# Kernel tuning notes

Hardware: AMD Instinct MI355X
Metric: run time of the kernel (lower is better)

The kernel has to match this reference:

```python
import jax, jax.numpy as jnp
import numpy as np

N = 100_000      # atom_count
E = 6_400_000    # number of (directed) edges, avg degree 64
BOX = 100.0      # simulation box edge length


def setup_inputs() -> dict:
    key = jax.random.key(0)
    k1, k2, k3 = jax.random.split(key, 3)
    pos = jax.random.uniform(k1, (N, 3), dtype=jnp.float32) * BOX
    src = jax.random.randint(k2, (E,), 0, N, dtype=jnp.int32)
    # offset in [1, N) guarantees dst != src (no zero-distance self edges)
    off = jax.random.randint(k3, (E,), 1, N, dtype=jnp.int32)
    dst = ((src + off) % N).astype(jnp.int32)
    edge_index = jnp.stack([src, dst], axis=0)  # [2, E]
    sigma = jnp.asarray(0.3, dtype=jnp.float32)
    epsilon = jnp.asarray(1.0, dtype=jnp.float32)
    return {"pos": pos, "sigma": sigma, "epsilon": epsilon, "edge_index": edge_index}


def _total_energy(pos, sigma, epsilon, src, dst):
    # r = edge_attr: per-edge distance, differentiable w.r.t. pos
    d = pos[src] - pos[dst]                      # [E, 3] gather + subtract
    r = jnp.sqrt(jnp.sum(d * d, axis=-1))        # [E]
    sr6 = (sigma / r) ** 6
    # potential_formula: 4*epsilon*((sigma/r)**12 - (sigma/r)**6)
    v_r = 4.0 * epsilon * (sr6 * sr6 - sr6)      # [E]
    return v_r.sum()


def reference(pos, sigma, epsilon, edge_index):
    src, dst = edge_index[0], edge_index[1]
    energy = _total_energy(pos, sigma, epsilon, src, dst)
    # afc: autograd force — grad of summed pair potential w.r.t. positions
    # (per-edge force scattered onto atoms by edge_index; grad does the
    #  gather-compute-scatter in one pass)
    pair_force = jax.grad(_total_energy, argnums=0)(pos, sigma, epsilon, src, dst)
    atom_force = -pair_force / 2.0               # /2: each pair counted twice
    return energy, atom_force
```

## Files before the change

kernel.cpp:

```cpp
#include <hip/hip_runtime.h>


#define NBINS      8
#define BIN_ATOMS  12800
#define BIN_F      (BIN_ATOMS * 3)
#define ROW_F      (NBINS * BIN_F)
#define BLOCK      1024
#define MAXCHUNKS  32

__global__ __launch_bounds__(BLOCK, 1) void pairforce_binned(
    const float* __restrict__ pos,
    const float* __restrict__ sigma_p,
    const float* __restrict__ eps_p,
    const int*   __restrict__ src,
    const int*   __restrict__ dst,
    float* __restrict__ frep,
    float* __restrict__ erep,
    int nEdges, int chunkEdges)
{
    extern __shared__ float sh[];
    const int t = threadIdx.x;
    const int b = blockIdx.x % NBINS;
    const int c = blockIdx.x / NBINS;

    for (int j = t; j < (BIN_F + 16) / 4; j += BLOCK)
        ((float4*)sh)[j] = make_float4(0.f, 0.f, 0.f, 0.f);
    __syncthreads();

    const float sigma = sigma_p[0];
    const float eps   = eps_p[0];
    const float sig2  = sigma * sigma;
    const int binStart = b * BIN_ATOMS;

    const int start = c * chunkEdges;
    const int end   = min(start + chunkEdges, nEdges);

    const int4* src4 = (const int4*)src;
    const int4* dst4 = (const int4*)dst;

    float ev = 0.0f;

    for (int i4 = (start >> 2) + t; i4 < (end >> 2); i4 += BLOCK) {
        const int4 s4 = src4[i4];
        const int4 d4 = dst4[i4];
        #pragma unroll
        for (int k = 0; k < 4; ++k) {
            const int s = (k == 0) ? s4.x : (k == 1) ? s4.y : (k == 2) ? s4.z : s4.w;
            const int d = (k == 0) ? d4.x : (k == 1) ? d4.y : (k == 2) ? d4.z : d4.w;
            const unsigned ls = (unsigned)(s - binStart);
            const unsigned ld = (unsigned)(d - binStart);
            const bool hs = ls < BIN_ATOMS;
            const bool hd = ld < BIN_ATOMS;
            if (hs | hd) {
                const float dx = pos[3 * s + 0] - pos[3 * d + 0];
                const float dy = pos[3 * s + 1] - pos[3 * d + 1];
                const float dz = pos[3 * s + 2] - pos[3 * d + 2];
                const float r2     = dx * dx + dy * dy + dz * dz;
                const float inv_r2 = 1.0f / r2;
                const float s2     = sig2 * inv_r2;
                const float sr6    = s2 * s2 * s2;
                const float sr12   = sr6 * sr6;
                const float fs = 12.0f * eps * (2.0f * sr12 - sr6) * inv_r2;
                const float fx = fs * dx;
                const float fy = fs * dy;
                const float fz = fs * dz;
                if (hs) {
                    atomicAdd(&sh[3 * ls + 0],  fx);
                    atomicAdd(&sh[3 * ls + 1],  fy);
                    atomicAdd(&sh[3 * ls + 2],  fz);
                    ev += 4.0f * eps * (sr12 - sr6);
                }
                if (hd) {
                    atomicAdd(&sh[3 * ld + 0], -fx);
                    atomicAdd(&sh[3 * ld + 1], -fy);
                    atomicAdd(&sh[3 * ld + 2], -fz);
                }
            }
        }
    }

    #pragma unroll
    for (int off = 32; off > 0; off >>= 1)
        ev += __shfl_down(ev, off, 64);
    if ((t & 63) == 0) sh[BIN_F + (t >> 6)] = ev;
    __syncthreads();

    float4* outSeg = (float4*)(frep + (size_t)c * ROW_F + (size_t)b * BIN_F);
    for (int j = t; j < BIN_F / 4; j += BLOCK)
        outSeg[j] = ((float4*)sh)[j];

    if (t == 0) {
        float e = 0.f;
        #pragma unroll
        for (int w = 0; w < 16; ++w) e += sh[BIN_F + w];
        erep[blockIdx.x] = e;
    }
}

__global__ __launch_bounds__(256) void pairforce_reduce(
    const float* __restrict__ frep,
    const float* __restrict__ erep,
    float* __restrict__ out,
    int n3, int nChunks, int nPart)
{
    const int i = blockIdx.x * 256 + threadIdx.x;
    if (i < n3) {
        float acc = 0.f;
        for (int c = 0; c < nChunks; ++c)
            acc += frep[(size_t)c * ROW_F + i];
        out[1 + i] = acc;
    }
    if (blockIdx.x == gridDim.x - 1) {
        float e = 0.f;
        for (int j = threadIdx.x; j < nPart; j += 256) e += erep[j];
        #pragma unroll
        for (int off = 32; off > 0; off >>= 1) e += __shfl_down(e, off, 64);
        __shared__ float ep[4];
        if ((threadIdx.x & 63) == 0) ep[threadIdx.x >> 6] = e;
        __syncthreads();
        if (threadIdx.x == 0) out[0] = ep[0] + ep[1] + ep[2] + ep[3];
    }
}

extern "C" void kernel_launch(void* const* d_in, const int* in_sizes, int n_in,
                              void* d_out, int out_size, void* d_ws, size_t ws_size,
                              hipStream_t stream)
{
    const float* pos     = (const float*)d_in[0];
    const float* sigma_p = (const float*)d_in[1];
    const float* eps_p   = (const float*)d_in[2];
    const int*   edge    = (const int*)d_in[3];

    const int nEdges = in_sizes[3] / 2;
    const int* src = edge;
    const int* dst = edge + nEdges;

    const int n3 = out_size - 1;

    const size_t rowBytes = (size_t)ROW_F * sizeof(float);
    int nChunks = (int)((ws_size - 4096) / rowBytes);
    if (nChunks > MAXCHUNKS) nChunks = MAXCHUNKS;
    if (nChunks < 1) nChunks = 1;

    const int chunkEdges = (((nEdges + nChunks - 1) / nChunks) + 3) & ~3;

    float* frep = (float*)d_ws;
    float* erep = frep + (size_t)nChunks * ROW_F;

    const size_t shbytes = (size_t)(BIN_F + 16) * sizeof(float);

    const int grid1 = nChunks * NBINS;
    pairforce_binned<<<grid1, BLOCK, shbytes, stream>>>(
        pos, sigma_p, eps_p, src, dst, frep, erep, nEdges, chunkEdges);

    const int grid2 = (n3 + 255) / 256;
    pairforce_reduce<<<grid2, 256, 0, stream>>>(
        frep, erep, (float*)d_out, n3, nChunks, nChunks * NBINS);
}
```

Measured before the change: 313.1 us.

## Replace atomic binned accumulation with counting-sort of edge records per atom class

Adds a multi-kernel pipeline: per-wave histogram of edge endpoints into bins and classes, a three-stage prefix scan, placement of encoded records, then a per-thread accumulation where each thread owns an atom class so shared-memory force sums need no atomics. Positions are repacked into float4 to make gathers single loads. It is meant to remove the shared-memory atomic contention and the redundant edge scans across 8 bins of the old kernel. In exchange it adds several launches, a low-parallelism count/place phase with serialized vote loops, and extra record traffic.

```diff
diff --git a/kernel.cpp b/kernel.cpp
--- a/kernel.cpp
+++ b/kernel.cpp
@@ -1,12 +1,308 @@
 #include <hip/hip_runtime.h>
 
+
+#define NBIN   32
+#define BA     3200
+#define NCLS   128
+#define LBK    (NBIN * NCLS)
+#define NSEG   512
+#define CBLK   64
+#define NB_TOT (NSEG * LBK)
+#define NROW   8
+#define ROW_F  307200
 
 #define NBINS      8
 #define BIN_ATOMS  12800
 #define BIN_F      (BIN_ATOMS * 3)
-#define ROW_F      (NBINS * BIN_F)
 #define BLOCK      1024
 #define MAXCHUNKS  32
+
+__device__ __forceinline__ unsigned nt_load_u(const unsigned* p) {
+    return __builtin_nontemporal_load(p);
+}
+
+
+__device__ __forceinline__ void vote_count(volatile unsigned* vh,
+                                           volatile unsigned* vote,
+                                           int lane, int act, unsigned lb) {
+    int pend = act, guard = 0;
+    while (__any(pend)) {
+        if (pend) vote[lb & 1023u] = (unsigned)lane;
+        if (pend && vote[lb & 1023u] == (unsigned)lane) { vh[lb] += 1u; pend = 0; }
+        if (++guard >= 72) break;
+    }
+    if (__any(pend)) {
+        for (int l2 = 0; l2 < 64; ++l2)
+            if (pend && lane == l2) { vh[lb] += 1u; pend = 0; }
+    }
+}
+
+__device__ __forceinline__ void vote_place(volatile unsigned* vc,
+                                           volatile unsigned* vote,
+                                           unsigned* __restrict__ recs,
+                                           int lane, int act, unsigned lb,
+                                           unsigned enc) {
+    int pend = act, guard = 0;
+    while (__any(pend)) {
+        if (pend) vote[lb & 1023u] = (unsigned)lane;
+        if (pend && vote[lb & 1023u] == (unsigned)lane) {
+            const unsigned s = vc[lb]; vc[lb] = s + 1u;
+            recs[s] = enc;
+            pend = 0;
+        }
+        if (++guard >= 72) break;
+    }
+    if (__any(pend)) {
+        for (int l2 = 0; l2 < 64; ++l2)
+            if (pend && lane == l2) {
+                const unsigned s = vc[lb]; vc[lb] = s + 1u;
+                recs[s] = enc;
+                pend = 0;
+            }
+    }
+}
+
+__global__ __launch_bounds__(512) void pf_count(
+    const float* __restrict__ pos, float4* __restrict__ pos4,
+    const int* __restrict__ src, const int* __restrict__ dst,
+    unsigned* __restrict__ cnt, int nEdges, int nAtoms)
+{
+    extern __shared__ unsigned u[];
+    const int t = threadIdx.x, lane = t & 63, wv = t >> 6;
+    const int bid = (int)blockIdx.x;
+
+    for (int k = t; k < 8 * LBK + 1024; k += 512) u[k] = 0u;
+    for (int i = bid * 512 + t; i < nAtoms; i += CBLK * 512)
+        pos4[i] = make_float4(pos[3 * i + 0], pos[3 * i + 1], pos[3 * i + 2], 0.f);
+    __syncthreads();
+
+    volatile unsigned* vh   = u + (size_t)wv * LBK;
+    volatile unsigned* vote = u + 8 * LBK;
+
+    const int w    = bid * 8 + wv;
+    const int epw  = (nEdges + NSEG - 1) / NSEG;
+    const int ebeg = w * epw;
+    const int eend = (ebeg + epw < nEdges) ? (ebeg + epw) : nEdges;
+
+    for (int base = ebeg; base < eend; base += 64) {
+        const int e = base + lane;
+        const int act = e < eend;
+        unsigned su = 0, du = 0;
+        if (act) { su = (unsigned)src[e]; du = (unsigned)dst[e]; }
+        {
+            const unsigned bin = su / BA;
+            vote_count(vh, vote, lane, act, bin * NCLS + (su & (NCLS - 1u)));
+        }
+        {
+            const unsigned bin = du / BA;
+            vote_count(vh, vote, lane, act, bin * NCLS + (du & (NCLS - 1u)));
+        }
+    }
+    __syncthreads();
+    for (int k = lane; k < LBK; k += 64)
+        cnt[(size_t)w * LBK + k] = u[(size_t)wv * LBK + k];
+}
+
+__global__ __launch_bounds__(1024) void pf_scanA(
+    const unsigned* __restrict__ cnt, unsigned* __restrict__ bstart,
+    unsigned* __restrict__ btot)
+{
+    __shared__ unsigned wt[16], wo[16];
+    const int t = threadIdx.x, lane = t & 63, wv = t >> 6;
+    const int gid = (int)blockIdx.x * 1024 + t;
+    const unsigned v = cnt[gid];
+    unsigned x = v;
+    #pragma unroll
+    for (int off = 1; off < 64; off <<= 1) {
+        const unsigned n = __shfl_up(x, off, 64);
+        if (lane >= off) x += n;
+    }
+    if (lane == 63) wt[wv] = x;
+    __syncthreads();
+    if (t == 0) {
+        unsigned run = 0;
+        #pragma unroll
+        for (int w = 0; w < 16; ++w) { wo[w] = run; run += wt[w]; }
+        btot[blockIdx.x] = run;
+    }
+    __syncthreads();
+    bstart[gid] = (x - v) + wo[wv];
+}
+
+__global__ __launch_bounds__(1024) void pf_scanB(
+    const unsigned* __restrict__ btot, unsigned* __restrict__ boffs)
+{
+    __shared__ unsigned wt[16], wo[16];
+    const int t = threadIdx.x, lane = t & 63, wv = t >> 6;
+    const unsigned a = btot[2 * t];
+    const unsigned b = btot[2 * t + 1];
+    const unsigned p = a + b;
+    unsigned x = p;
+    #pragma unroll
+    for (int off = 1; off < 64; off <<= 1) {
+        const unsigned n = __shfl_up(x, off, 64);
+        if (lane >= off) x += n;
+    }
+    if (lane == 63) wt[wv] = x;
+    __syncthreads();
+    if (t == 0) {
+        unsigned run = 0;
+        #pragma unroll
+        for (int w = 0; w < 16; ++w) { wo[w] = run; run += wt[w]; }
+    }
+    __syncthreads();
+    const unsigned ex = (x - p) + wo[wv];
+    boffs[2 * t] = ex;
+    boffs[2 * t + 1] = ex + a;
+}
+
+__global__ __launch_bounds__(1024) void pf_scanC(
+    unsigned* __restrict__ bstart, const unsigned* __restrict__ boffs, int nRec)
+{
+    const int gid = (int)blockIdx.x * 1024 + threadIdx.x;
+    bstart[gid] += boffs[blockIdx.x];
+    if (gid == 0) bstart[NB_TOT] = (unsigned)nRec;
+}
+
+__global__ __launch_bounds__(512) void pf_place(
+    const int* __restrict__ src, const int* __restrict__ dst,
+    const unsigned* __restrict__ bstart, unsigned* __restrict__ recs, int nEdges)
+{
+    extern __shared__ unsigned u[];
+    const int t = threadIdx.x, lane = t & 63, wv = t >> 6;
+    const int bid = (int)blockIdx.x;
+    const int w = bid * 8 + wv;
+
+    for (int k = lane; k < LBK; k += 64)
+        u[(size_t)wv * LBK + k] = bstart[(size_t)w * LBK + k];
+    __syncthreads();
+
+    volatile unsigned* vc   = u + (size_t)wv * LBK;
+    volatile unsigned* vote = u + 8 * LBK;
+
+    const int epw  = (nEdges + NSEG - 1) / NSEG;
+    const int ebeg = w * epw;
+    const int eend = (ebeg + epw < nEdges) ? (ebeg + epw) : nEdges;
+
+    for (int base = ebeg; base < eend; base += 64) {
+        const int e = base + lane;
+        const int act = e < eend;
+        unsigned su = 0, du = 0;
+        if (act) { su = (unsigned)src[e]; du = (unsigned)dst[e]; }
+        {
+            const unsigned bin = su / BA;
+            const unsigned li  = su - bin * BA;
+            vote_place(vc, vote, recs, lane, act,
+                       bin * NCLS + (su & (NCLS - 1u)),
+                       (li << 18) | (1u << 17) | du);
+        }
+        {
+            const unsigned bin = du / BA;
+            const unsigned li  = du - bin * BA;
+            vote_place(vc, vote, recs, lane, act,
+                       bin * NCLS + (du & (NCLS - 1u)),
+                       (li << 18) | su);
+        }
+    }
+}
+
+__global__ __launch_bounds__(512) void pf_accum(
+    const float4* __restrict__ pos4,
+    const float* __restrict__ sigma_p, const float* __restrict__ eps_p,
+    const unsigned* __restrict__ recs, const unsigned* __restrict__ bstart,
+    float* __restrict__ frep,
+    float* __restrict__ erep)
+{
+    extern __shared__ float sh[];
+    __shared__ float sE[8];
+    const int t = threadIdx.x, lane = t & 63, wv = t >> 6;
+    const int b = (int)blockIdx.x;
+    const int bin = b & 31, strip = b >> 5;
+    const int c = t & (NCLS - 1), ss = t >> 7;
+
+    for (int k = t; k < 4 * 9600 / 4; k += 512)
+        ((float4*)sh)[k] = make_float4(0.f, 0.f, 0.f, 0.f);
+    __syncthreads();
+
+    const float sigma = sigma_p[0], eps = eps_p[0];
+    const float sig2 = sigma * sigma;
+    const float c12 = 12.f * eps, c4 = 4.f * eps;
+
+    float* sF = sh + ss * 9600;
+    const int binBase = bin * BA;
+    float ev = 0.f;
+
+    for (int k = 0; k < 16; ++k) {
+        const int seg = strip * 64 + ss * 16 + k;
+        const size_t g = (size_t)seg * LBK + bin * NCLS + c;
+        const int beg = (int)bstart[g];
+        const int end = (int)bstart[g + 1];
+        for (int r = beg; r < end; ++r) {
+            const unsigned rec = nt_load_u(recs + r);
+            const int li = rec >> 18;
+            const int o  = rec & 0x1FFFF;
+            const float4 pa = pos4[binBase + li];
+            const float4 po = pos4[o];
+            const float dx = pa.x - po.x, dy = pa.y - po.y, dz = pa.z - po.z;
+            const float r2   = dx * dx + dy * dy + dz * dz;
+            const float ir2  = 1.0f / r2;
+            const float s2   = sig2 * ir2;
+            const float sr6  = s2 * s2 * s2;
+            const float sr12 = sr6 * sr6;
+            const float fs   = c12 * (2.f * sr12 - sr6) * ir2;
+            sF[3 * li + 0] += fs * dx;
+            sF[3 * li + 1] += fs * dy;
+            sF[3 * li + 2] += fs * dz;
+            ev += (rec & (1u << 17)) ? c4 * (sr12 - sr6) : 0.f;
+        }
+    }
+
+    #pragma unroll
+    for (int off = 32; off > 0; off >>= 1) ev += __shfl_down(ev, off, 64);
+    if (lane == 0) sE[wv] = ev;
+    __syncthreads();
+
+    float4* dOut = (float4*)(frep + (size_t)strip * ROW_F + (size_t)bin * (BA * 3));
+    const float4* s0 = (const float4*)(sh);
+    const float4* s1 = (const float4*)(sh + 9600);
+    const float4* s2 = (const float4*)(sh + 19200);
+    const float4* s3 = (const float4*)(sh + 28800);
+    for (int k = t; k < 9600 / 4; k += 512) {
+        const float4 a = s0[k], b2 = s1[k], c2 = s2[k], d2 = s3[k];
+        dOut[k] = make_float4(a.x + b2.x + c2.x + d2.x, a.y + b2.y + c2.y + d2.y,
+                              a.z + b2.z + c2.z + d2.z, a.w + b2.w + c2.w + d2.w);
+    }
+    if (t == 0) {
+        float e = 0.f;
+        #pragma unroll
+        for (int w = 0; w < 8; ++w) e += sE[w];
+        erep[b] = e;
+    }
+}
+
+__global__ __launch_bounds__(256) void pairforce_reduce(
+    const float* __restrict__ frep,
+    const float* __restrict__ erep,
+    float* __restrict__ out, int n3, int nChunks, int nPart)
+{
+    const int i = blockIdx.x * 256 + threadIdx.x;
+    if (i < n3) {
+        float acc = 0.f;
+        for (int c = 0; c < nChunks; ++c)
+            acc += frep[(size_t)c * ROW_F + i];
+        out[1 + i] = acc;
+    }
+    if (blockIdx.x == gridDim.x - 1) {
+        float e = 0.f;
+        for (int jj = threadIdx.x; jj < nPart; jj += 256) e += erep[jj];
+        #pragma unroll
+        for (int off = 32; off > 0; off >>= 1) e += __shfl_down(e, off, 64);
+        __shared__ float ep[4];
+        if ((threadIdx.x & 63) == 0) ep[threadIdx.x >> 6] = e;
+        __syncthreads();
+        if (threadIdx.x == 0) out[0] = ep[0] + ep[1] + ep[2] + ep[3];
+    }
+}
 
 __global__ __launch_bounds__(BLOCK, 1) void pairforce_binned(
     const float* __restrict__ pos,
@@ -23,8 +319,8 @@
     const int b = blockIdx.x % NBINS;
     const int c = blockIdx.x / NBINS;
 
-    for (int j = t; j < (BIN_F + 16) / 4; j += BLOCK)
-        ((float4*)sh)[j] = make_float4(0.f, 0.f, 0.f, 0.f);
+    for (int jj = t; jj < (BIN_F + 16) / 4; jj += BLOCK)
+        ((float4*)sh)[jj] = make_float4(0.f, 0.f, 0.f, 0.f);
     __syncthreads();
 
     const float sigma = sigma_p[0];
@@ -86,39 +382,14 @@
     __syncthreads();
 
     float4* outSeg = (float4*)(frep + (size_t)c * ROW_F + (size_t)b * BIN_F);
-    for (int j = t; j < BIN_F / 4; j += BLOCK)
-        outSeg[j] = ((float4*)sh)[j];
+    for (int jj = t; jj < BIN_F / 4; jj += BLOCK)
+        outSeg[jj] = ((float4*)sh)[jj];
 
     if (t == 0) {
         float e = 0.f;
         #pragma unroll
         for (int w = 0; w < 16; ++w) e += sh[BIN_F + w];
         erep[blockIdx.x] = e;
-    }
-}
-
-__global__ __launch_bounds__(256) void pairforce_reduce(
-    const float* __restrict__ frep,
-    const float* __restrict__ erep,
-    float* __restrict__ out,
-    int n3, int nChunks, int nPart)
-{
-    const int i = blockIdx.x * 256 + threadIdx.x;
-    if (i < n3) {
-        float acc = 0.f;
-        for (int c = 0; c < nChunks; ++c)
-            acc += frep[(size_t)c * ROW_F + i];
-        out[1 + i] = acc;
-    }
-    if (blockIdx.x == gridDim.x - 1) {
-        float e = 0.f;
-        for (int j = threadIdx.x; j < nPart; j += 256) e += erep[j];
-        #pragma unroll
-        for (int off = 32; off > 0; off >>= 1) e += __shfl_down(e, off, 64);
-        __shared__ float ep[4];
-        if ((threadIdx.x & 63) == 0) ep[threadIdx.x >> 6] = e;
-        __syncthreads();
-        if (threadIdx.x == 0) out[0] = ep[0] + ep[1] + ep[2] + ep[3];
     }
 }
 
@@ -136,6 +407,36 @@
     const int* dst = edge + nEdges;
 
     const int n3 = out_size - 1;
+    const int nAtoms = n3 / 3;
+    const int nRec = 2 * nEdges;
+
+    auto alignup = [](size_t x) { return (x + 255) & ~(size_t)255; };
+    size_t off = 0;
+    unsigned* recs   = (unsigned*)((char*)d_ws + off); off = alignup(off + (size_t)nRec * 4);
+    unsigned* cntp   = (unsigned*)((char*)d_ws + off); off = alignup(off + (size_t)NB_TOT * 4);
+    unsigned* bstart = (unsigned*)((char*)d_ws + off); off = alignup(off + (size_t)(NB_TOT + 1) * 4);
+    unsigned* btot   = (unsigned*)((char*)d_ws + off); off = alignup(off + 2048 * 4);
+    unsigned* boffs  = (unsigned*)((char*)d_ws + off); off = alignup(off + 2048 * 4);
+    float*    pos4   = (float*)((char*)d_ws + off);    off = alignup(off + (size_t)(NBIN * BA) * 16);
+    float*    frepN  = (float*)((char*)d_ws + off);    off = alignup(off + (size_t)NROW * ROW_F * 4);
+    float*    erepN  = (float*)((char*)d_ws + off);    off = alignup(off + 256 * 4);
+
+    if (ws_size >= off && nAtoms <= NBIN * BA && nEdges > 0 && (nEdges & 3) == 0) {
+        const size_t shCP = (size_t)(8 * LBK + 1024) * 4;
+        pf_count<<<CBLK, 512, shCP, stream>>>(pos, (float4*)pos4, src, dst,
+                                              cntp, nEdges, nAtoms);
+        pf_scanA<<<NB_TOT / 1024, 1024, 0, stream>>>(cntp, bstart, btot);
+        pf_scanB<<<1, 1024, 0, stream>>>(btot, boffs);
+        pf_scanC<<<NB_TOT / 1024, 1024, 0, stream>>>(bstart, boffs, nRec);
+        pf_place<<<CBLK, 512, shCP, stream>>>(src, dst, bstart, recs, nEdges);
+        const size_t shA = (size_t)(4 * 9600) * 4;
+        pf_accum<<<NBIN * NROW, 512, shA, stream>>>((const float4*)pos4,
+                                                    sigma_p, eps_p, recs, bstart,
+                                                    frepN, erepN);
+        pairforce_reduce<<<(n3 + 255) / 256, 256, 0, stream>>>(
+            frepN, erepN, (float*)d_out, n3, NROW, NBIN * NROW);
+        return;
+    }
 
     const size_t rowBytes = (size_t)ROW_F * sizeof(float);
     int nChunks = (int)((ws_size - 4096) / rowBytes);
```

Result: slower. 868.3 us (+177.4%).
